# Optimization experiments

Measured on AMD Instinct MI355X. Metric: run time of the kernel, lower is better.

## Reference

```python
import jax, jax.numpy as jnp
import numpy as np
from jax import lax

# ----- config (mirrors CochlearModel defaults) -----
SR = 48000
NCH = 64
Q = 9.26
ORDER = 4
FMIN, FMAX = 100.0, 8000.0
TAU_HC_MS = 0.5
REFRAC = 1.0
ADAPT_RATE = 0.01
TH0 = 0.1
DT = 1.0 / SR
# LowPassFilter: cutoff = 1000/(2*pi*tau_hc) -> tau = tau_hc/1000 s; alpha = dt/(dt+tau)
ALPHA = DT / (DT + TAU_HC_MS / 1000.0)


def _make_kernels():
    # ERB-spaced center frequencies, gammatone impulse responses, peak-normalized.
    erb = lambda f: 21.4 * np.log10(0.00437 * f + 1.0)
    ierb = lambda e: (10.0 ** (e / 21.4) - 1.0) / 0.00437
    cfs = ierb(np.linspace(erb(FMIN), erb(FMAX), NCH))
    irs = []
    for cf in cfs:
        bw = cf / Q
        n = int(4.0 / (2.0 * np.pi * bw) * SR)  # duration = 4*tau
        t = np.arange(n) * DT
        ir = t ** (ORDER - 1) * np.exp(-2.0 * np.pi * bw * t) * np.cos(2.0 * np.pi * cf * t)
        irs.append((ir / np.abs(ir).max()).astype(np.float32))
    L = max(len(ir) for ir in irs)
    K = np.zeros((NCH, L), np.float32)
    for i, ir in enumerate(irs):
        # front-pad: with left pad L-1 on x, this reproduces torch's per-filter
        # causal conv (left pad len_i-1) exactly for every channel.
        K[i, L - len(ir):] = ir
    return jnp.asarray(K)


def setup_inputs() -> dict:
    key = jax.random.key(0)
    audio = jax.random.normal(key, (4, SR), dtype=jnp.float32)
    return {"audio_signal": audio, "kernels": _make_kernels()}


def _filterbank(x, kernels):
    # x: [B, T] -> [B, C, T]; causal cross-correlation = torch F.conv1d with left pad
    L = kernels.shape[1]
    xp = jnp.pad(x, ((0, 0), (L - 1, 0)))[:, None, :]  # [B,1,T+L-1]
    return lax.conv_general_dilated(xp, kernels[:, None, :], (1,), 'VALID',
                                    dimension_numbers=('NCW', 'OIW', 'NCW'))


def _process_ear(audio, kernels, carry):
    resp = _filterbank(audio, kernels)               # [B,C,T]
    rect = jax.nn.relu(jnp.moveaxis(resp, 2, 0))     # [T,B,C]

    def step(c, xt):
        s, tim, thr = c
        # hair-cell first-order low-pass (EMA)
        s = ALPHA * xt + (1.0 - ALPHA) * s           # [B,C]
        refr = tim > 0.0                             # [C] (shared across batch, as in source)
        spk = ((s > thr[None, :]) & (~refr)[None, :]).astype(s.dtype)
        tim = jnp.where(jnp.any(spk > 0.0, axis=0), REFRAC, tim)
        tim = jnp.maximum(tim - 1.0, 0.0)
        # adaptive threshold: rise with batch-mean spiking, leak toward baseline
        thr = thr + ADAPT_RATE * jnp.mean(spk, axis=0) + ADAPT_RATE * (TH0 - thr)
        return (s, tim, thr), (s, spk)

    carry, (hair, spk) = lax.scan(step, carry, rect)
    return carry, jnp.swapaxes(hair, 0, 1), jnp.swapaxes(spk, 0, 1)  # [B,T,C]


def reference(audio_signal, kernels):
    B = audio_signal.shape[0]
    dt = audio_signal.dtype
    # LPF / refractory / threshold buffers persist across the two ears (stateful buffers in source)
    carry = (jnp.zeros((B, NCH), dt), jnp.zeros((NCH,), dt), jnp.full((NCH,), TH0, dt))
    spikes, resps = [], []
    for _ in range(2):  # mono input duplicated to 2 ears, processed sequentially
        carry, hair, spk = _process_ear(audio_signal, kernels, carry)
        spikes.append(spk)
        resps.append(hair)
    spike_trains = jnp.concatenate(spikes, axis=-1)  # [B, T, 2*C]
    channel_responses = jnp.stack(resps, axis=1)     # [B, 2, T, C]
    return spike_trains, channel_responses
```

## Files before the change

### kernel.cpp

```cpp
#include <hip/hip_runtime.h>
#include <hip/hip_bf16.h>

#define T_LEN 48000
#define NCH   64
#define NB    4
#define CT    96
#define WU    128
#define TTILE 256

static constexpr double DTd    = 1.0 / 48000.0;
static constexpr double ALPHAd = DTd / (DTd + 0.0005);
static constexpr float  AF     = (float)ALPHAd;
static constexpr float  OMF    = (float)(1.0 - ALPHAd);

typedef __attribute__((ext_vector_type(8))) short bf16x8;
typedef __attribute__((ext_vector_type(4))) float f32x4;
typedef bf16x8 bf16x8_u __attribute__((aligned(4)));

static __device__ __forceinline__ unsigned short f2bf(float f) {
    __hip_bfloat16 h = __float2bfloat16(f);
    unsigned short u; __builtin_memcpy(&u, &h, 2);
    return u;
}

__global__ __launch_bounds__(256) void prep_all(
        const float* __restrict__ x, const float* __restrict__ Km,
        int* __restrict__ kstart, unsigned short* __restrict__ xc,
        unsigned short* __restrict__ Afrag,
        int L, int SMAX8, int SMAXA, int PAD, int XCAP) {
    const int role = blockIdx.y;
    if (role < 4) {
        const int g = role, s = blockIdx.x;
        if (s >= SMAX8) return;
        __shared__ int smin;
        if (threadIdx.x == 0) smin = L - 1;
        __syncthreads();
        const float* row = Km + (size_t)(g * 16) * L;
        int local = L - 1;
        for (int i = threadIdx.x; i < L; i += 256)
            if (row[i] != 0.0f) { local = i; break; }
        atomicMin(&smin, local);
        __syncthreads();
        const int ks = smin;
        if (s == 0 && threadIdx.x == 0) kstart[g * 16] = ks;
        if (threadIdx.x < 64) {
            const int lane = threadIdx.x;
            const int Lg = L - ks;
            const int r = lane & 15, khi = lane >> 4;
            const float* kr = Km + (size_t)(g * 16 + r) * L + ks;
            const size_t off = ((size_t)(g * SMAXA + s) * 64 + lane) * 8;
            #pragma unroll
            for (int jj = 0; jj < 8; ++jj) {
                const int q = 32 * s + 8 * khi + jj;
                Afrag[off + jj] = (q < Lg) ? f2bf(kr[q]) : (unsigned short)0;
            }
        }
    } else {
        const int idx = blockIdx.x * 256 + threadIdx.x;
        if (idx >= NB * XCAP) return;
        const int b = idx / XCAP, j = idx % XCAP;
        const float* xb = x + (size_t)b * T_LEN;
        const int t0 = j - PAD, t1 = t0 + 1;
        xc[((size_t)b * 2 + 0) * XCAP + j] = (t0 >= 0 && t0 < T_LEN) ? f2bf(xb[t0]) : (unsigned short)0;
        xc[((size_t)b * 2 + 1) * XCAP + j] = (t1 >= 0 && t1 < T_LEN) ? f2bf(xb[t1]) : (unsigned short)0;
    }
}

__global__ __launch_bounds__(256, 2) void conv_mfma(
        const unsigned short* __restrict__ xc, const unsigned short* __restrict__ Afrag,
        const int* __restrict__ kstart, unsigned short* __restrict__ rectT,
        int L, int SMAXA, int PAD, int XCAP) {
    const int lane = threadIdx.x & 63;
    const int w    = threadIdx.x >> 6;
    const int g    = blockIdx.y;
    const int t0   = blockIdx.x * TTILE;
    const int ks   = kstart[g * 16];
    const int Lg   = L - ks;
    const int nst8 = (((Lg + 31) >> 5) + 7) & ~7;
    const int nl   = lane & 15, khi = lane >> 4;
    const int i0   = t0 + nl + 8 * khi - (Lg - 1);
    const int p    = i0 & 1;
    const unsigned short* xp  = xc + ((size_t)(w * 2 + p)) * XCAP + (PAD + i0 - p);
    const unsigned short* apw = Afrag + ((size_t)(g * SMAXA) + 2 * w) * 512 + (size_t)lane * 8;

    __shared__ __align__(16) short smem[256 * 72];
    short* As = smem;

    f32x4 acc[16];
    #pragma unroll
    for (int j = 0; j < 16; ++j) acc[j] = (f32x4){0.f, 0.f, 0.f, 0.f};
    bf16x8 bx[16];
    #pragma unroll
    for (int j = 0; j < 16; ++j) bx[j] = *(const bf16x8_u*)(xp + 16 * j);

    {
        const bf16x8 s0 = *(const bf16x8*)(apw);
        const bf16x8 s1 = *(const bf16x8*)(apw + 512);
        *(bf16x8*)(&As[(2 * w)     * 512 + lane * 8]) = s0;
        *(bf16x8*)(&As[(2 * w + 1) * 512 + lane * 8]) = s1;
    }
    __syncthreads();

#define GROUP(areg, U)                                                                   \
    acc[0] = __builtin_amdgcn_mfma_f32_16x16x32_bf16(areg, bx[(2*(U))     & 15], acc[0], 0, 0, 0); \
    acc[1] = __builtin_amdgcn_mfma_f32_16x16x32_bf16(areg, bx[(2*(U) + 1) & 15], acc[1], 0, 0, 0); \
    bx[(2*(U))     & 15] = *(const bf16x8_u*)(xp + 256 + 32 * (U));                      \
    bx[(2*(U) + 1) & 15] = *(const bf16x8_u*)(xp + 272 + 32 * (U));                      \
    _Pragma("unroll")                                                                    \
    for (int j = 2; j < 16; ++j)                                                         \
        acc[j] = __builtin_amdgcn_mfma_f32_16x16x32_bf16(areg, bx[(2*(U) + j) & 15], acc[j], 0, 0, 0);

    int q = 0;
    for (int s = 0; s < nst8; s += 8) {
        const bf16x8 n0 = *(const bf16x8*)(apw + (size_t)(s + 8) * 512);
        const bf16x8 n1 = *(const bf16x8*)(apw + (size_t)(s + 9) * 512);
        const short* Ab = As + q * 4096;
        {
            const bf16x8 a0 = *(const bf16x8*)(&Ab[       lane * 8]);
            const bf16x8 a1 = *(const bf16x8*)(&Ab[ 512 + lane * 8]);
            const bf16x8 a2 = *(const bf16x8*)(&Ab[1024 + lane * 8]);
            const bf16x8 a3 = *(const bf16x8*)(&Ab[1536 + lane * 8]);
            GROUP(a0, 0)
            GROUP(a1, 1)
            GROUP(a2, 2)
            GROUP(a3, 3)
        }
        {
            const bf16x8 a4 = *(const bf16x8*)(&Ab[2048 + lane * 8]);
            const bf16x8 a5 = *(const bf16x8*)(&Ab[2560 + lane * 8]);
            const bf16x8 a6 = *(const bf16x8*)(&Ab[3072 + lane * 8]);
            const bf16x8 a7 = *(const bf16x8*)(&Ab[3584 + lane * 8]);
            GROUP(a4, 4)
            GROUP(a5, 5)
            GROUP(a6, 6)
            GROUP(a7, 7)
        }
        *(bf16x8*)(&As[(q ^ 1) * 4096 + (2 * w)     * 512 + lane * 8]) = n0;
        *(bf16x8*)(&As[(q ^ 1) * 4096 + (2 * w + 1) * 512 + lane * 8]) = n1;
        __syncthreads();
        q ^= 1;
        xp += 256;
    }
#undef GROUP

    short* S = smem;
    #pragma unroll
    for (int j = 0; j < 16; ++j) {
        #pragma unroll
        for (int v = 0; v < 4; ++v)
            S[(16 * j + nl) * 72 + (4 * khi + v) * 4 + w] =
                (short)f2bf(fmaxf(acc[j][v], 0.f));
    }
    __syncthreads();
    {
        const int rr = threadIdx.x >> 3, ch = threadIdx.x & 7;
        #pragma unroll
        for (int it = 0; it < 8; ++it) {
            const int r = it * 32 + rr;
            if (t0 + r < T_LEN) {
                const uint4 v = *(const uint4*)(&S[r * 72 + 8 * ch]);
                *(uint4*)(rectT + ((size_t)(t0 + r)) * 256 + 64 * g + 8 * ch) = v;
            }
        }
    }
}

static __device__ __forceinline__ float bfw(unsigned int w, int odd) {
    return __uint_as_float(odd ? (w & 0xFFFF0000u) : (w << 16));
}

__device__ __forceinline__ void scan_step(float r0, float r1, float r2, float r3,
        int u, bool store, int c, float* __restrict__ out0, float* __restrict__ out1,
        float& s0, float& s1, float& s2, float& s3, float& thr) {
    s0 = AF * r0 + OMF * s0;
    s1 = AF * r1 + OMF * s1;
    s2 = AF * r2 + OMF * s2;
    s3 = AF * r3 + OMF * s3;
    const float k0 = (s0 > thr) ? 1.0f : 0.0f;
    const float k1 = (s1 > thr) ? 1.0f : 0.0f;
    const float k2 = (s2 > thr) ? 1.0f : 0.0f;
    const float k3 = (s3 > thr) ? 1.0f : 0.0f;
    const float cnt = (k0 + k1) + (k2 + k3);
    thr = thr + 0.01f * (cnt * 0.25f) + 0.01f * (0.1f - thr);
    if (store) {
        const int e  = (u >= T_LEN) ? 1 : 0;
        const int tt = u - (e ? T_LEN : 0);
        const int o1 = ((e * T_LEN + tt) << 6) + c;
        out1[o1]                   = s0;
        out1[o1 + 2 * T_LEN * NCH] = s1;
        out1[o1 + 4 * T_LEN * NCH] = s2;
        out1[o1 + 6 * T_LEN * NCH] = s3;
        const int o0 = (tt << 7) + (e << 6) + c;
        out0[o0]                   = k0;
        out0[o0 + T_LEN * 128]     = k1;
        out0[o0 + 2 * T_LEN * 128] = k2;
        out0[o0 + 3 * T_LEN * 128] = k3;
    }
}

#define LOAD_G16(buf, ug) do {                                                       \
    const int tt_ = ((ug) < T_LEN) ? (ug) : ((ug) - T_LEN);                          \
    const unsigned short* bp_ = rectT + (size_t)tt_ * 256 + c * 4;                   \
    _Pragma("unroll")                                                                \
    for (int q_ = 0; q_ < 16; ++q_) buf[q_] = *(const uint2*)(bp_ + q_ * 256);       \
} while (0)

#define PROC_G16(buf, ug) do {                                                       \
    _Pragma("unroll")                                                                \
    for (int q_ = 0; q_ < 16; ++q_) {                                                \
        const float r0_ = bfw(buf[q_].x, 0);                                         \
        const float r1_ = bfw(buf[q_].x, 1);                                         \
        const float r2_ = bfw(buf[q_].y, 0);                                         \
        const float r3_ = bfw(buf[q_].y, 1);                                         \
        scan_step(r0_, r1_, r2_, r3_, (ug) + q_, STORE, c, out0, out1, s0, s1, s2, s3, thr); \
    }                                                                                \
} while (0)

template <bool STORE>
__device__ __forceinline__ void scan_range(int from, int to, int c,
        const unsigned short* __restrict__ rectT, float* __restrict__ out0, float* __restrict__ out1,
        float& s0, float& s1, float& s2, float& s3, float& thr) {
    if (from >= to) return;
    uint2 bufA[16], bufB[16];
    LOAD_G16(bufA, from);
    for (int ug = from; ug < to; ug += 32) {
        LOAD_G16(bufB, ug + 16);
        PROC_G16(bufA, ug);
        if (ug + 32 < to) LOAD_G16(bufA, ug + 32);
        PROC_G16(bufB, ug + 16);
    }
}

__global__ __launch_bounds__(256) void scan_kernel(const unsigned short* __restrict__ rectT,
                                                   float* __restrict__ out) {
    const int k = blockIdx.x * 4 + (int)(threadIdx.x >> 6);
    if (k >= (2 * T_LEN) / CT) return;
    const int c    = threadIdx.x & 63;
    const int u0   = k * CT;
    const int uend = u0 + CT;
    const int w0   = (u0 >= WU) ? (u0 - WU) : 0;
    float s0 = 0.f, s1 = 0.f, s2 = 0.f, s3 = 0.f, thr = 0.1f;
    float* out0 = out;
    float* out1 = out + (size_t)NB * T_LEN * 2 * NCH;
    scan_range<false>(w0, u0,   c, rectT, out0, out1, s0, s1, s2, s3, thr);
    scan_range<true >(u0, uend, c, rectT, out0, out1, s0, s1, s2, s3, thr);
}

extern "C" void kernel_launch(void* const* d_in, const int* in_sizes, int n_in,
                              void* d_out, int out_size, void* d_ws, size_t ws_size,
                              hipStream_t stream) {
    const float* x  = (const float*)d_in[0];
    const float* Km = (const float*)d_in[1];
    const int L     = in_sizes[1] / NCH;
    const int SMAX  = (L + 31) / 32;
    const int SMAX8 = (SMAX + 7) & ~7;
    const int SMAXA = SMAX8 + 8;
    const int PAD   = (L + 1) & ~1;
    const int XCAP  = PAD + T_LEN + 1024;

    char* w = (char*)d_ws;
    int* kstart = (int*)w;
    unsigned short* xc = (unsigned short*)(w + 512);
    const size_t xc_bytes = (size_t)NB * 2 * XCAP * 2;
    unsigned short* Afrag = (unsigned short*)(w + 512 + ((xc_bytes + 15) & ~(size_t)15));
    const size_t a_bytes = (size_t)4 * SMAXA * 64 * 8 * 2;
    unsigned short* rectT = (unsigned short*)((char*)Afrag + ((a_bytes + 15) & ~(size_t)15));

    const int pxBlocks = (NB * XCAP + 255) / 256;
    dim3 pgrid(pxBlocks > SMAX8 ? pxBlocks : SMAX8, 5);
    prep_all<<<pgrid, 256, 0, stream>>>(x, Km, kstart, xc, Afrag, L, SMAX8, SMAXA, PAD, XCAP);
    conv_mfma<<<dim3((T_LEN + TTILE - 1) / TTILE, 4), 256, 0, stream>>>(
        xc, Afrag, kstart, rectT, L, SMAXA, PAD, XCAP);
    const int nchunks = (2 * T_LEN) / CT;
    scan_kernel<<<(nchunks + 3) / 4, 256, 0, stream>>>(rectT, (float*)d_out);
}
```

Baseline: 84.49 us.

## Pipeline conv and scan across five mixed launches over time slices

Merges the convolution and scan kernels into one mixed kernel whose blocks do either a conv tile or scan waves. The launch is split into five nodes, so that scan chunks whose inputs earlier conv slices already produced run alongside later conv slices. The goal is to overlap the latency-bound scan with the compute-bound conv instead of running them back to back. It adds four extra launches, hard-coded slice tables tied to T_LEN/CT/TTILE, and a dependence on the scan warmup window (WU) staying within already-computed data.

```diff
diff --git a/kernel.cpp b/kernel.cpp
--- a/kernel.cpp
+++ b/kernel.cpp
@@ -66,14 +66,13 @@
     }
 }
 
-__global__ __launch_bounds__(256, 2) void conv_mfma(
+__device__ __forceinline__ void conv_block(
         const unsigned short* __restrict__ xc, const unsigned short* __restrict__ Afrag,
         const int* __restrict__ kstart, unsigned short* __restrict__ rectT,
-        int L, int SMAXA, int PAD, int XCAP) {
+        int L, int SMAXA, int PAD, int XCAP, int g, int t0) {
+    __shared__ __align__(16) short smem[256 * 72];
     const int lane = threadIdx.x & 63;
     const int w    = threadIdx.x >> 6;
-    const int g    = blockIdx.y;
-    const int t0   = blockIdx.x * TTILE;
     const int ks   = kstart[g * 16];
     const int Lg   = L - ks;
     const int nst8 = (((Lg + 31) >> 5) + 7) & ~7;
@@ -82,8 +81,6 @@
     const int p    = i0 & 1;
     const unsigned short* xp  = xc + ((size_t)(w * 2 + p)) * XCAP + (PAD + i0 - p);
     const unsigned short* apw = Afrag + ((size_t)(g * SMAXA) + 2 * w) * 512 + (size_t)lane * 8;
-
-    __shared__ __align__(16) short smem[256 * 72];
     short* As = smem;
 
     f32x4 acc[16];
@@ -231,11 +228,8 @@
     }
 }
 
-__global__ __launch_bounds__(256) void scan_kernel(const unsigned short* __restrict__ rectT,
-                                                   float* __restrict__ out) {
-    const int k = blockIdx.x * 4 + (int)(threadIdx.x >> 6);
-    if (k >= (2 * T_LEN) / CT) return;
-    const int c    = threadIdx.x & 63;
+__device__ __forceinline__ void scan_wave(const unsigned short* __restrict__ rectT,
+                                          float* __restrict__ out, int k, int c) {
     const int u0   = k * CT;
     const int uend = u0 + CT;
     const int w0   = (u0 >= WU) ? (u0 - WU) : 0;
@@ -244,6 +238,24 @@
     float* out1 = out + (size_t)NB * T_LEN * 2 * NCH;
     scan_range<false>(w0, u0,   c, rectT, out0, out1, s0, s1, s2, s3, thr);
     scan_range<true >(u0, uend, c, rectT, out0, out1, s0, s1, s2, s3, thr);
+}
+
+__global__ __launch_bounds__(256, 2) void mixed_kernel(
+        const unsigned short* __restrict__ xc, const unsigned short* __restrict__ Afrag,
+        const int* __restrict__ kstart, unsigned short* __restrict__ rectT,
+        float* __restrict__ out,
+        int L, int SMAXA, int PAD, int XCAP,
+        int ncv, int ct0, int lo1, int n1, int lo2, int n2) {
+    const int bx = (int)blockIdx.x;
+    if (bx < ncv * 4) {
+        conv_block(xc, Afrag, kstart, rectT, L, SMAXA, PAD, XCAP,
+                   bx / ncv, (ct0 + bx % ncv) * TTILE);
+    } else {
+        const int sidx = (bx - ncv * 4) * 4 + (int)(threadIdx.x >> 6);
+        if (sidx >= n1 + n2) return;
+        const int k = (sidx < n1) ? (lo1 + sidx) : (lo2 + (sidx - n1));
+        scan_wave(rectT, out, k, (int)(threadIdx.x & 63));
+    }
 }
 
 extern "C" void kernel_launch(void* const* d_in, const int* in_sizes, int n_in,
@@ -269,8 +281,21 @@
     const int pxBlocks = (NB * XCAP + 255) / 256;
     dim3 pgrid(pxBlocks > SMAX8 ? pxBlocks : SMAX8, 5);
     prep_all<<<pgrid, 256, 0, stream>>>(x, Km, kstart, xc, Afrag, L, SMAX8, SMAXA, PAD, XCAP);
-    conv_mfma<<<dim3((T_LEN + TTILE - 1) / TTILE, 4), 256, 0, stream>>>(
-        xc, Afrag, kstart, rectT, L, SMAXA, PAD, XCAP);
-    const int nchunks = (2 * T_LEN) / CT;
-    scan_kernel<<<(nchunks + 3) / 4, 256, 0, stream>>>(rectT, (float*)d_out);
-}
+
+    struct NodeCfg { int ncv, ct0, lo1, n1, lo2, n2; };
+    const NodeCfg nodes[5] = {
+        { 47,   0,   0,   0,   0,   0 },
+        { 47,  47,   0, 125, 502, 123 },
+        { 47,  94, 125, 125, 625, 125 },
+        { 47, 141, 250, 126, 750, 126 },
+        {  0,   0, 376, 126, 876, 124 },
+    };
+    for (int i = 0; i < 5; ++i) {
+        const NodeCfg& nd = nodes[i];
+        const int nscan_blocks = (nd.n1 + nd.n2 + 3) / 4;
+        const int grid = nd.ncv * 4 + nscan_blocks;
+        mixed_kernel<<<grid, 256, 0, stream>>>(xc, Afrag, kstart, rectT, (float*)d_out,
+                                               L, SMAXA, PAD, XCAP,
+                                               nd.ncv, nd.ct0, nd.lo1, nd.n1, nd.lo2, nd.n2);
+    }
+}
```

Measured after the change: 152.4 us. 1.8x slower.

## Load filter fragments directly from global into registers, drop LDS staging and barriers

Applied to the files above, without the earlier changes.

Each wave now reads the filter A-fragments for every k-step straight from global memory into registers, with a four-fragment register prefetch, instead of cooperatively staging them into a double-buffered shared-memory buffer. This removes the per-iteration __syncthreads and the LDS round trip. In exchange every wave issues four times the global/L2 loads for the filter data, and the launch bound no longer requests two blocks per CU, so register allocation may change occupancy. A barrier is added before reusing shared memory for the output transpose.

```diff
diff --git a/kernel.cpp b/kernel.cpp
--- a/kernel.cpp
+++ b/kernel.cpp
@@ -66,7 +66,7 @@
     }
 }
 
-__global__ __launch_bounds__(256, 2) void conv_mfma(
+__global__ __launch_bounds__(256) void conv_mfma(
         const unsigned short* __restrict__ xc, const unsigned short* __restrict__ Afrag,
         const int* __restrict__ kstart, unsigned short* __restrict__ rectT,
         int L, int SMAXA, int PAD, int XCAP) {
@@ -80,11 +80,10 @@
     const int nl   = lane & 15, khi = lane >> 4;
     const int i0   = t0 + nl + 8 * khi - (Lg - 1);
     const int p    = i0 & 1;
-    const unsigned short* xp  = xc + ((size_t)(w * 2 + p)) * XCAP + (PAD + i0 - p);
-    const unsigned short* apw = Afrag + ((size_t)(g * SMAXA) + 2 * w) * 512 + (size_t)lane * 8;
-
-    __shared__ __align__(16) short smem[256 * 72];
-    short* As = smem;
+    const unsigned short* xp = xc + ((size_t)(w * 2 + p)) * XCAP + (PAD + i0 - p);
+    const unsigned short* ap = Afrag + (size_t)(g * SMAXA) * 512 + (size_t)lane * 8;
+
+    __shared__ __align__(16) short S[256 * 72];
 
     f32x4 acc[16];
     #pragma unroll
@@ -93,13 +92,10 @@
     #pragma unroll
     for (int j = 0; j < 16; ++j) bx[j] = *(const bf16x8_u*)(xp + 16 * j);
 
-    {
-        const bf16x8 s0 = *(const bf16x8*)(apw);
-        const bf16x8 s1 = *(const bf16x8*)(apw + 512);
-        *(bf16x8*)(&As[(2 * w)     * 512 + lane * 8]) = s0;
-        *(bf16x8*)(&As[(2 * w + 1) * 512 + lane * 8]) = s1;
-    }
-    __syncthreads();
+    bf16x8 A0 = *(const bf16x8*)(ap);
+    bf16x8 A1 = *(const bf16x8*)(ap + 512);
+    bf16x8 A2 = *(const bf16x8*)(ap + 1024);
+    bf16x8 A3 = *(const bf16x8*)(ap + 1536);
 
 #define GROUP(areg, U)                                                                   \
     acc[0] = __builtin_amdgcn_mfma_f32_16x16x32_bf16(areg, bx[(2*(U))     & 15], acc[0], 0, 0, 0); \
@@ -110,40 +106,29 @@
     for (int j = 2; j < 16; ++j)                                                         \
         acc[j] = __builtin_amdgcn_mfma_f32_16x16x32_bf16(areg, bx[(2*(U) + j) & 15], acc[j], 0, 0, 0);
 
-    int q = 0;
     for (int s = 0; s < nst8; s += 8) {
-        const bf16x8 n0 = *(const bf16x8*)(apw + (size_t)(s + 8) * 512);
-        const bf16x8 n1 = *(const bf16x8*)(apw + (size_t)(s + 9) * 512);
-        const short* Ab = As + q * 4096;
-        {
-            const bf16x8 a0 = *(const bf16x8*)(&Ab[       lane * 8]);
-            const bf16x8 a1 = *(const bf16x8*)(&Ab[ 512 + lane * 8]);
-            const bf16x8 a2 = *(const bf16x8*)(&Ab[1024 + lane * 8]);
-            const bf16x8 a3 = *(const bf16x8*)(&Ab[1536 + lane * 8]);
-            GROUP(a0, 0)
-            GROUP(a1, 1)
-            GROUP(a2, 2)
-            GROUP(a3, 3)
-        }
-        {
-            const bf16x8 a4 = *(const bf16x8*)(&Ab[2048 + lane * 8]);
-            const bf16x8 a5 = *(const bf16x8*)(&Ab[2560 + lane * 8]);
-            const bf16x8 a6 = *(const bf16x8*)(&Ab[3072 + lane * 8]);
-            const bf16x8 a7 = *(const bf16x8*)(&Ab[3584 + lane * 8]);
-            GROUP(a4, 4)
-            GROUP(a5, 5)
-            GROUP(a6, 6)
-            GROUP(a7, 7)
-        }
-        *(bf16x8*)(&As[(q ^ 1) * 4096 + (2 * w)     * 512 + lane * 8]) = n0;
-        *(bf16x8*)(&As[(q ^ 1) * 4096 + (2 * w + 1) * 512 + lane * 8]) = n1;
-        __syncthreads();
-        q ^= 1;
+        const unsigned short* ab = ap + (size_t)s * 512;
+        const bf16x8 N0 = *(const bf16x8*)(ab + 2048);
+        const bf16x8 N1 = *(const bf16x8*)(ab + 2560);
+        const bf16x8 N2 = *(const bf16x8*)(ab + 3072);
+        const bf16x8 N3 = *(const bf16x8*)(ab + 3584);
+        GROUP(A0, 0)
+        GROUP(A1, 1)
+        GROUP(A2, 2)
+        GROUP(A3, 3)
+        A0 = *(const bf16x8*)(ab + 4096);
+        A1 = *(const bf16x8*)(ab + 4608);
+        A2 = *(const bf16x8*)(ab + 5120);
+        A3 = *(const bf16x8*)(ab + 5632);
+        GROUP(N0, 4)
+        GROUP(N1, 5)
+        GROUP(N2, 6)
+        GROUP(N3, 7)
         xp += 256;
     }
 #undef GROUP
 
-    short* S = smem;
+    __syncthreads();
     #pragma unroll
     for (int j = 0; j < 16; ++j) {
         #pragma unroll
```

Result: slower. 92.10 us (+9.0%).
